# Kernel tuning notes

Measured on AMD Instinct MI355X. Metric: run time of the kernel, lower is better.

The kernel has to match this reference:

```python
import jax, jax.numpy as jnp
import numpy as np


def _pad_kernel_like(kernel_oc0, H, W, ks):
    # torch: F.pad(k,(p,p,p,p)) then if shape mismatch F.pad(k,(0,1,0,1))
    p = (H - ks) // 2
    extra = H - (ks + 2 * p)  # 0 or 1
    return jnp.pad(kernel_oc0, ((0, 0), (p, p + extra), (p, p + extra)))


def setup_inputs() -> dict:
    key = jax.random.key(0)
    k1, k2 = jax.random.split(key)
    B, C, H, W = 8, 16, 128, 128
    O, KS = 32, 9
    x = jax.random.normal(k1, (B, C, H, W), dtype=jnp.float32)
    # kaiming_uniform-ish init scale
    fan_in = C * KS * KS
    bound = float(np.sqrt(6.0 / fan_in))
    kernel = jax.random.uniform(k2, (O, C, KS, KS), dtype=jnp.float32,
                                minval=-bound, maxval=bound)
    return {"x": x, "kernel": kernel}


def reference(x, kernel):
    # x: [B,C,H,W] float32, kernel: [O,C,ks,ks] float32
    B, C, H, W = x.shape
    O, ks = kernel.shape[0], kernel.shape[-1]
    # Faithful to original bug: only kernel[:, 0] is used for every input channel.
    k = _pad_kernel_like(kernel[:, 0], H, W, ks)  # [O,H,W]
    # 4f optical FFT convolution: ifftshift -> FFT -> multiply -> IFFT -> fftshift -> |.|
    Fx = jnp.fft.fft2(jnp.fft.ifftshift(x, axes=(-2, -1)))   # [B,C,H,W] complex64
    Fk = jnp.fft.fft2(jnp.fft.ifftshift(k, axes=(-2, -1)))   # [O,H,W]   complex64
    prod = Fx[:, None, :, :, :] * Fk[None, :, None, :, :]    # [B,O,C,H,W]
    field = jnp.fft.fftshift(jnp.fft.ifft2(prod), axes=(-2, -1))
    out_pc = jnp.abs(field)                                  # per-(out,in)-channel intensity
    return out_pc.sum(axis=2)                                # [B,O,H,W]
```

## Files before the change

kernel.cpp:

```cpp
#include <hip/hip_runtime.h>


typedef __attribute__((ext_vector_type(8)))  short  short8;
typedef __attribute__((ext_vector_type(4)))  float  float4v;
typedef __attribute__((ext_vector_type(4)))  unsigned int uint4v;

#define XR_ROWS 138
#define XR_RDW  72
#define XR_CH_DW (XR_ROWS * XR_RDW)
#define XR_TOT_DW (128 * XR_CH_DW)
#define BPRE_OFF ((size_t)128 * XR_ROWS * 288)
#define CHB 3168
#define PREP_BLOCKS 2048
#define PREP_STRIDE (PREP_BLOCKS * 256)

__device__ __forceinline__ unsigned int f2bf(float f) {
    union { float f; unsigned int u; } a; a.f = f;
    unsigned int u = a.u;
    u += 0x7fffu + ((u >> 16) & 1u);
    return u >> 16;
}

#if __has_builtin(__builtin_amdgcn_alignbit)
#define ALIGN16(hi_, lo_) __builtin_amdgcn_alignbit((hi_), (lo_), 16)
#else
#define ALIGN16(hi_, lo_) \
    (unsigned int)((((unsigned long long)(hi_) << 32) | (lo_)) >> 16)
#endif

#define FRAG_EVEN(q_) __builtin_bit_cast(short8, (uint4v){                    \
        wnd[(q_)+0], wnd[(q_)+1], wnd[(q_)+2], wnd[(q_)+3]})
#define FRAG_ODD(q_)  __builtin_bit_cast(short8, (uint4v){                    \
        ALIGN16(wnd[(q_)+1], wnd[(q_)+0]),                                    \
        ALIGN16(wnd[(q_)+2], wnd[(q_)+1]),                                    \
        ALIGN16(wnd[(q_)+3], wnd[(q_)+2]),                                    \
        ALIGN16(wnd[(q_)+4], wnd[(q_)+3])})

__device__ __forceinline__ void gload_lds16(const void* g, void* l) {
    __builtin_amdgcn_global_load_lds(
        (const __attribute__((address_space(1))) unsigned int*)g,
        (__attribute__((address_space(3))) unsigned int*)l, 16, 0, 0);
}

__global__ __launch_bounds__(256)
void optical_prep_69698729279498(const float* __restrict__ x,
                                 const float* __restrict__ kern,
                                 unsigned int* __restrict__ xr,
                                 uint4v* __restrict__ bpre) {
    if (blockIdx.x == PREP_BLOCKS) {
        const int l = threadIdx.x;
        if (l < 64) {
            const int lk = l & 15;
            const int g2 = l >> 4;
            for (int oh = 0; oh < 2; ++oh) {
                const int o = oh * 16 + lk;
                for (int ck = 0; ck < 5; ++ck) {
                    const int ti  = 2 * ck + (g2 >> 1);
                    const int tj0 = (g2 & 1) * 8;
                    unsigned int pk[4];
#pragma unroll
                    for (int ee = 0; ee < 4; ++ee) {
                        int tj_a = tj0 + 2 * ee, tj_b = tj_a + 1;
                        float va = (ti <= 8 && tj_a <= 8) ? kern[o * 1296 + ti * 9 + tj_a] : 0.f;
                        float vb = (ti <= 8 && tj_b <= 8) ? kern[o * 1296 + ti * 9 + tj_b] : 0.f;
                        pk[ee] = f2bf(va) | (f2bf(vb) << 16);
                    }
                    bpre[(oh * 5 + ck) * 64 + l] = (uint4v){pk[0], pk[1], pk[2], pk[3]};
                }
            }
        }
        return;
    }
    for (int idx = blockIdx.x * 256 + threadIdx.x; idx < XR_TOT_DW;
         idx += PREP_STRIDE) {
        int bc  = idx / XR_CH_DW;
        int rem = idx - bc * XR_CH_DW;
        int r   = rem / XR_RDW;
        int ccd = rem - r * XR_RDW;
        int cc  = 2 * ccd;
        const float* xp = x + (bc << 14) + ((r & 127) << 7);
        float v0 = xp[(132 - cc) & 127];
        float v1 = xp[(131 - cc) & 127];
        xr[idx] = f2bf(v0) | (f2bf(v1) << 16);
    }
}

__global__ __launch_bounds__(512, 4)
void optical_conv_69698729279498(const unsigned int* __restrict__ xr,
                                 const uint4v* __restrict__ bpre,
                                 float* __restrict__ out) {
    __shared__ __align__(16) unsigned short ldsb[16 * (CHB / 2)];

    const int tid = threadIdx.x;
    const int l   = tid & 63;
    const int w   = tid >> 6;
    const int oh  = w & 1;
    const int rh  = (w >> 1) & 1;
    const int cg  = w >> 2;
    const int i0  = blockIdx.x * 2;
    const int b   = blockIdx.y;

    const int lk   = l & 15;
    const int g    = (l >> 4) & 1;
    const int hi32 = l >> 5;
    const int g2   = l >> 4;
    const int o    = oh * 16 + lk;

    const int wstart = (i0 >= 4) ? (i0 - 4) : (i0 + 124);
    const char* xr8 = (const char*)xr;
#pragma unroll
    for (int cw = 0; cw < 2; ++cw) {
        const int ch = 2 * w + cw;
        const char* src = xr8 + ((size_t)((b * 16 + ch) * XR_ROWS + wstart)) * 288;
        char* dst = (char*)ldsb + ch * CHB;
        gload_lds16(src + 0 * 1024 + l * 16, dst + 0 * 1024);
        gload_lds16(src + 1 * 1024 + l * 16, dst + 1 * 1024);
        gload_lds16(src + 2 * 1024 + l * 16, dst + 2 * 1024);
        if (l < 6)
            gload_lds16(src + 3072 + l * 16, dst + 3072);
    }

    short8 Bf[5];
#pragma unroll
    for (int ck = 0; ck < 5; ++ck)
        Bf[ck] = __builtin_bit_cast(short8, bpre[(oh * 5 + ck) * 64 + l]);

    __syncthreads();

    float4v acc[8];
#pragma unroll
    for (int p = 0; p < 8; ++p) acc[p] = (float4v){0.f, 0.f, 0.f, 0.f};
    const float4v zero4 = (float4v){0.f, 0.f, 0.f, 0.f};

    const char* lb = (const char*)ldsb
                   + (240 - 16 * lk + 16 * g) + (1 - hi32 + rh) * 288
                   + cg * 8 * CHB;

    for (int c = 0; c < 8; ++c) {
        float4v D[8];
#pragma unroll
        for (int ck = 0; ck < 5; ++ck) {
            const char* p = lb + (8 - 2 * ck) * 288;
            uint4v w0 = *(const uint4v*)p;
            uint4v w1 = *(const uint4v*)(p + 16);
            unsigned int wnd[8] = {w0.x, w0.y, w0.z, w0.w,
                                   w1.x, w1.y, w1.z, w1.w};
            short8 f0 = FRAG_ODD(3),  f1 = FRAG_EVEN(3);
            short8 f2 = FRAG_ODD(2),  f3 = FRAG_EVEN(2);
            short8 f4 = FRAG_ODD(1),  f5 = FRAG_EVEN(1);
            short8 f6 = FRAG_ODD(0),  f7 = FRAG_EVEN(0);
            D[0] = __builtin_amdgcn_mfma_f32_16x16x32_bf16(f0, Bf[ck], ck ? D[0] : zero4, 0, 0, 0);
            D[1] = __builtin_amdgcn_mfma_f32_16x16x32_bf16(f1, Bf[ck], ck ? D[1] : zero4, 0, 0, 0);
            D[2] = __builtin_amdgcn_mfma_f32_16x16x32_bf16(f2, Bf[ck], ck ? D[2] : zero4, 0, 0, 0);
            D[3] = __builtin_amdgcn_mfma_f32_16x16x32_bf16(f3, Bf[ck], ck ? D[3] : zero4, 0, 0, 0);
            D[4] = __builtin_amdgcn_mfma_f32_16x16x32_bf16(f4, Bf[ck], ck ? D[4] : zero4, 0, 0, 0);
            D[5] = __builtin_amdgcn_mfma_f32_16x16x32_bf16(f5, Bf[ck], ck ? D[5] : zero4, 0, 0, 0);
            D[6] = __builtin_amdgcn_mfma_f32_16x16x32_bf16(f6, Bf[ck], ck ? D[6] : zero4, 0, 0, 0);
            D[7] = __builtin_amdgcn_mfma_f32_16x16x32_bf16(f7, Bf[ck], ck ? D[7] : zero4, 0, 0, 0);
        }
#pragma unroll
        for (int p = 0; p < 8; ++p)
#pragma unroll
            for (int e = 0; e < 4; ++e) acc[p][e] += fabsf(D[p][e]);
        lb += CHB;
    }

    __syncthreads();
    float* red = (float*)ldsb;
    const int rbase = ((w & 3) * 64 + l) * 36;
    if (cg == 1) {
#pragma unroll
        for (int p = 0; p < 8; ++p)
            *(float4v*)&red[rbase + 4 * p] = acc[p];
    }
    __syncthreads();
    if (cg == 0) {
#pragma unroll
        for (int p = 0; p < 8; ++p) {
            float4v r = *(const float4v*)&red[rbase + 4 * p];
#pragma unroll
            for (int e = 0; e < 4; ++e) acc[p][e] += r[e];
        }
        const int i = i0 + rh;
        float* ob = out + ((((size_t)(b * 32 + o)) * 128 + i) << 7);
#pragma unroll
        for (int e = 0; e < 4; ++e) {
            float4v lo = (float4v){acc[0][e], acc[1][e], acc[2][e], acc[3][e]};
            float4v hi = (float4v){acc[4][e], acc[5][e], acc[6][e], acc[7][e]};
            *(float4v*)&ob[32 * g2 + 8 * e]     = lo;
            *(float4v*)&ob[32 * g2 + 8 * e + 4] = hi;
        }
    }
}

extern "C" void kernel_launch(void* const* d_in, const int* in_sizes, int n_in,
                              void* d_out, int out_size, void* d_ws, size_t ws_size,
                              hipStream_t stream) {
    const float* x = (const float*)d_in[0];
    const float* kern = (const float*)d_in[1];
    float* out = (float*)d_out;
    unsigned int* xr = (unsigned int*)d_ws;
    uint4v* bpre = (uint4v*)((char*)d_ws + BPRE_OFF);

    hipLaunchKernelGGL(optical_prep_69698729279498, dim3(PREP_BLOCKS + 1),
                       dim3(256), 0, stream, x, kern, xr, bpre);
    hipLaunchKernelGGL(optical_conv_69698729279498, dim3(64, 8), dim3(512),
                       0, stream, xr, bpre, out);
}
```

Measured before the change: 95.31 us.

## Switch conv to 32x32x16 MFMA with LDS-staged coalesced output

Replaces the 16x16x32 bf16 MFMA tiling (5 K-chunks of row pairs) with 32x32x16 MFMA over all 9 kernel rows, covering all 32 output channels per wave. Blocks shrink to 256 threads with 4 channels loaded per wave, and the output is transposed through LDS so global stores are row-contiguous. The prep kernel gets a 2D grid without the division-heavy grid-stride loop. This trades zero-padded K waste and more MFMA instructions for fewer, larger MFMAs, at the cost of higher accumulator register pressure and an extra LDS pass.

```diff
diff --git a/kernel.cpp b/kernel.cpp
--- a/kernel.cpp
+++ b/kernel.cpp
@@ -2,17 +2,16 @@
 
 
 typedef __attribute__((ext_vector_type(8)))  short  short8;
+typedef __attribute__((ext_vector_type(16))) float  float16v;
 typedef __attribute__((ext_vector_type(4)))  float  float4v;
 typedef __attribute__((ext_vector_type(4)))  unsigned int uint4v;
 
 #define XR_ROWS 138
 #define XR_RDW  72
 #define XR_CH_DW (XR_ROWS * XR_RDW)
-#define XR_TOT_DW (128 * XR_CH_DW)
+#define XR_CH_B  (XR_CH_DW * 4)
 #define BPRE_OFF ((size_t)128 * XR_ROWS * 288)
 #define CHB 3168
-#define PREP_BLOCKS 2048
-#define PREP_STRIDE (PREP_BLOCKS * 256)
 
 __device__ __forceinline__ unsigned int f2bf(float f) {
     union { float f; unsigned int u; } a; a.f = f;
@@ -47,45 +46,36 @@
                                  const float* __restrict__ kern,
                                  unsigned int* __restrict__ xr,
                                  uint4v* __restrict__ bpre) {
-    if (blockIdx.x == PREP_BLOCKS) {
-        const int l = threadIdx.x;
-        if (l < 64) {
-            const int lk = l & 15;
-            const int g2 = l >> 4;
-            for (int oh = 0; oh < 2; ++oh) {
-                const int o = oh * 16 + lk;
-                for (int ck = 0; ck < 5; ++ck) {
-                    const int ti  = 2 * ck + (g2 >> 1);
-                    const int tj0 = (g2 & 1) * 8;
-                    unsigned int pk[4];
-#pragma unroll
-                    for (int ee = 0; ee < 4; ++ee) {
-                        int tj_a = tj0 + 2 * ee, tj_b = tj_a + 1;
-                        float va = (ti <= 8 && tj_a <= 8) ? kern[o * 1296 + ti * 9 + tj_a] : 0.f;
-                        float vb = (ti <= 8 && tj_b <= 8) ? kern[o * 1296 + ti * 9 + tj_b] : 0.f;
-                        pk[ee] = f2bf(va) | (f2bf(vb) << 16);
-                    }
-                    bpre[(oh * 5 + ck) * 64 + l] = (uint4v){pk[0], pk[1], pk[2], pk[3]};
-                }
-            }
-        }
-        return;
-    }
-    for (int idx = blockIdx.x * 256 + threadIdx.x; idx < XR_TOT_DW;
-         idx += PREP_STRIDE) {
-        int bc  = idx / XR_CH_DW;
-        int rem = idx - bc * XR_CH_DW;
-        int r   = rem / XR_RDW;
-        int ccd = rem - r * XR_RDW;
+    const int t = blockIdx.x * 256 + threadIdx.x;
+    const int bc = blockIdx.y;
+    const int rem = t - 9984;
+    if (t < XR_CH_DW) {
+        int r   = t / 72;
+        int ccd = t - r * 72;
         int cc  = 2 * ccd;
         const float* xp = x + (bc << 14) + ((r & 127) << 7);
         float v0 = xp[(132 - cc) & 127];
         float v1 = xp[(131 - cc) & 127];
-        xr[idx] = f2bf(v0) | (f2bf(v1) << 16);
-    }
-}
-
-__global__ __launch_bounds__(512, 4)
+        xr[(size_t)bc * XR_CH_DW + t] = f2bf(v0) | (f2bf(v1) << 16);
+    } else if (bc == 0 && rem >= 0 && rem < 64) {
+        const int l  = rem;
+        const int o  = l & 31;
+        const int hi = l >> 5;
+        for (int ti = 0; ti < 9; ++ti) {
+            unsigned int pk[4];
+#pragma unroll
+            for (int ee = 0; ee < 4; ++ee) {
+                int tj_a = 8 * hi + 2 * ee, tj_b = tj_a + 1;
+                float va = (tj_a <= 8) ? kern[o * 1296 + ti * 9 + tj_a] : 0.f;
+                float vb = (tj_b <= 8) ? kern[o * 1296 + ti * 9 + tj_b] : 0.f;
+                pk[ee] = f2bf(va) | (f2bf(vb) << 16);
+            }
+            bpre[ti * 64 + l] = (uint4v){pk[0], pk[1], pk[2], pk[3]};
+        }
+    }
+}
+
+__global__ __launch_bounds__(256, 2)
 void optical_conv_69698729279498(const unsigned int* __restrict__ xr,
                                  const uint4v* __restrict__ bpre,
                                  float* __restrict__ out) {
@@ -94,23 +84,20 @@
     const int tid = threadIdx.x;
     const int l   = tid & 63;
     const int w   = tid >> 6;
-    const int oh  = w & 1;
-    const int rh  = (w >> 1) & 1;
-    const int cg  = w >> 2;
+    const int ph  = w & 1;
+    const int cg  = w >> 1;
     const int i0  = blockIdx.x * 2;
     const int b   = blockIdx.y;
 
-    const int lk   = l & 15;
-    const int g    = (l >> 4) & 1;
-    const int hi32 = l >> 5;
-    const int g2   = l >> 4;
-    const int o    = oh * 16 + lk;
+    const int jm  = l & 15;
+    const int rl  = (l >> 4) & 1;
+    const int hi  = l >> 5;
 
     const int wstart = (i0 >= 4) ? (i0 - 4) : (i0 + 124);
     const char* xr8 = (const char*)xr;
 #pragma unroll
-    for (int cw = 0; cw < 2; ++cw) {
-        const int ch = 2 * w + cw;
+    for (int cw = 0; cw < 4; ++cw) {
+        const int ch = 4 * w + cw;
         const char* src = xr8 + ((size_t)((b * 16 + ch) * XR_ROWS + wstart)) * 288;
         char* dst = (char*)ldsb + ch * CHB;
         gload_lds16(src + 0 * 1024 + l * 16, dst + 0 * 1024);
@@ -120,75 +107,91 @@
             gload_lds16(src + 3072 + l * 16, dst + 3072);
     }
 
-    short8 Bf[5];
-#pragma unroll
-    for (int ck = 0; ck < 5; ++ck)
-        Bf[ck] = __builtin_bit_cast(short8, bpre[(oh * 5 + ck) * 64 + l]);
-
-    __syncthreads();
-
-    float4v acc[8];
-#pragma unroll
-    for (int p = 0; p < 8; ++p) acc[p] = (float4v){0.f, 0.f, 0.f, 0.f};
-    const float4v zero4 = (float4v){0.f, 0.f, 0.f, 0.f};
+    short8 Bf[9];
+#pragma unroll
+    for (int ti = 0; ti < 9; ++ti)
+        Bf[ti] = __builtin_bit_cast(short8, bpre[ti * 64 + l]);
+
+    __syncthreads();
+
+    float16v acc[4];
+#pragma unroll
+    for (int pp = 0; pp < 4; ++pp)
+#pragma unroll
+        for (int e = 0; e < 16; ++e) acc[pp][e] = 0.f;
+    float16v zero16;
+#pragma unroll
+    for (int e = 0; e < 16; ++e) zero16[e] = 0.f;
 
     const char* lb = (const char*)ldsb
-                   + (240 - 16 * lk + 16 * g) + (1 - hi32 + rh) * 288
+                   + (240 - 16 * jm + 16 * hi) + (1 + rl) * 288
                    + cg * 8 * CHB;
 
     for (int c = 0; c < 8; ++c) {
-        float4v D[8];
-#pragma unroll
-        for (int ck = 0; ck < 5; ++ck) {
-            const char* p = lb + (8 - 2 * ck) * 288;
+        float16v D[4];
+#pragma unroll
+        for (int ti = 0; ti < 9; ++ti) {
+            const char* p = lb + (8 - ti) * 288;
             uint4v w0 = *(const uint4v*)p;
             uint4v w1 = *(const uint4v*)(p + 16);
             unsigned int wnd[8] = {w0.x, w0.y, w0.z, w0.w,
                                    w1.x, w1.y, w1.z, w1.w};
-            short8 f0 = FRAG_ODD(3),  f1 = FRAG_EVEN(3);
-            short8 f2 = FRAG_ODD(2),  f3 = FRAG_EVEN(2);
-            short8 f4 = FRAG_ODD(1),  f5 = FRAG_EVEN(1);
-            short8 f6 = FRAG_ODD(0),  f7 = FRAG_EVEN(0);
-            D[0] = __builtin_amdgcn_mfma_f32_16x16x32_bf16(f0, Bf[ck], ck ? D[0] : zero4, 0, 0, 0);
-            D[1] = __builtin_amdgcn_mfma_f32_16x16x32_bf16(f1, Bf[ck], ck ? D[1] : zero4, 0, 0, 0);
-            D[2] = __builtin_amdgcn_mfma_f32_16x16x32_bf16(f2, Bf[ck], ck ? D[2] : zero4, 0, 0, 0);
-            D[3] = __builtin_amdgcn_mfma_f32_16x16x32_bf16(f3, Bf[ck], ck ? D[3] : zero4, 0, 0, 0);
-            D[4] = __builtin_amdgcn_mfma_f32_16x16x32_bf16(f4, Bf[ck], ck ? D[4] : zero4, 0, 0, 0);
-            D[5] = __builtin_amdgcn_mfma_f32_16x16x32_bf16(f5, Bf[ck], ck ? D[5] : zero4, 0, 0, 0);
-            D[6] = __builtin_amdgcn_mfma_f32_16x16x32_bf16(f6, Bf[ck], ck ? D[6] : zero4, 0, 0, 0);
-            D[7] = __builtin_amdgcn_mfma_f32_16x16x32_bf16(f7, Bf[ck], ck ? D[7] : zero4, 0, 0, 0);
+            short8 f0, f1, f2, f3;
+            if (ph == 0) {
+                f0 = FRAG_ODD(3);  f1 = FRAG_EVEN(3);
+                f2 = FRAG_ODD(2);  f3 = FRAG_EVEN(2);
+            } else {
+                f0 = FRAG_ODD(1);  f1 = FRAG_EVEN(1);
+                f2 = FRAG_ODD(0);  f3 = FRAG_EVEN(0);
+            }
+            D[0] = __builtin_amdgcn_mfma_f32_32x32x16_bf16(f0, Bf[ti], ti ? D[0] : zero16, 0, 0, 0);
+            D[1] = __builtin_amdgcn_mfma_f32_32x32x16_bf16(f1, Bf[ti], ti ? D[1] : zero16, 0, 0, 0);
+            D[2] = __builtin_amdgcn_mfma_f32_32x32x16_bf16(f2, Bf[ti], ti ? D[2] : zero16, 0, 0, 0);
+            D[3] = __builtin_amdgcn_mfma_f32_32x32x16_bf16(f3, Bf[ti], ti ? D[3] : zero16, 0, 0, 0);
         }
 #pragma unroll
-        for (int p = 0; p < 8; ++p)
-#pragma unroll
-            for (int e = 0; e < 4; ++e) acc[p][e] += fabsf(D[p][e]);
+        for (int pp = 0; pp < 4; ++pp)
+#pragma unroll
+            for (int e = 0; e < 16; ++e) acc[pp][e] += fabsf(D[pp][e]);
         lb += CHB;
     }
 
     __syncthreads();
-    float* red = (float*)ldsb;
-    const int rbase = ((w & 3) * 64 + l) * 36;
+    float* otile = (float*)ldsb;
+    const int obase_l = (l & 31) * 129 + 32 * (l >> 5) + 4 * ph;
     if (cg == 1) {
 #pragma unroll
-        for (int p = 0; p < 8; ++p)
-            *(float4v*)&red[rbase + 4 * p] = acc[p];
+        for (int pp = 0; pp < 4; ++pp)
+#pragma unroll
+            for (int reg = 0; reg < 16; ++reg)
+                otile[obase_l + (reg >> 3) * 4128 + 8 * (reg & 3)
+                      + 64 * ((reg >> 2) & 1) + pp] = acc[pp][reg];
     }
     __syncthreads();
     if (cg == 0) {
 #pragma unroll
-        for (int p = 0; p < 8; ++p) {
-            float4v r = *(const float4v*)&red[rbase + 4 * p];
-#pragma unroll
-            for (int e = 0; e < 4; ++e) acc[p][e] += r[e];
-        }
-        const int i = i0 + rh;
-        float* ob = out + ((((size_t)(b * 32 + o)) * 128 + i) << 7);
-#pragma unroll
-        for (int e = 0; e < 4; ++e) {
-            float4v lo = (float4v){acc[0][e], acc[1][e], acc[2][e], acc[3][e]};
-            float4v hi = (float4v){acc[4][e], acc[5][e], acc[6][e], acc[7][e]};
-            *(float4v*)&ob[32 * g2 + 8 * e]     = lo;
-            *(float4v*)&ob[32 * g2 + 8 * e + 4] = hi;
+        for (int pp = 0; pp < 4; ++pp)
+#pragma unroll
+            for (int reg = 0; reg < 16; ++reg) {
+                const int idx = obase_l + (reg >> 3) * 4128 + 8 * (reg & 3)
+                              + 64 * ((reg >> 2) & 1) + pp;
+                otile[idx] += acc[pp][reg];
+            }
+    }
+    __syncthreads();
+
+    {
+        const int pair = tid >> 2;
+        const int q    = tid & 3;
+        const int r    = pair >> 5;
+        const int o    = pair & 31;
+        const float* src = otile + pair * 129 + q * 32;
+        float* dstg = out + ((((size_t)(b * 32 + o)) * 128 + (i0 + r)) << 7) + q * 32;
+#pragma unroll
+        for (int k4 = 0; k4 < 8; ++k4) {
+            float4v v = (float4v){src[4 * k4], src[4 * k4 + 1],
+                                  src[4 * k4 + 2], src[4 * k4 + 3]};
+            *(float4v*)&dstg[4 * k4] = v;
         }
     }
 }
@@ -202,8 +205,8 @@
     unsigned int* xr = (unsigned int*)d_ws;
     uint4v* bpre = (uint4v*)((char*)d_ws + BPRE_OFF);
 
-    hipLaunchKernelGGL(optical_prep_69698729279498, dim3(PREP_BLOCKS + 1),
+    hipLaunchKernelGGL(optical_prep_69698729279498, dim3(40, 128),
                        dim3(256), 0, stream, x, kern, xr, bpre);
-    hipLaunchKernelGGL(optical_conv_69698729279498, dim3(64, 8), dim3(512),
+    hipLaunchKernelGGL(optical_conv_69698729279498, dim3(64, 8), dim3(256),
                        0, stream, xr, bpre, out);
 }
```

After: 94.45 us. No clear change (-0.9%).
